# Optimization experiments

Hardware: AMD Instinct MI355X
Metric: run time of the kernel (lower is better)

The kernel has to match this reference:

```python
import jax, jax.numpy as jnp
import numpy as np

B, L, D, H = 4, 256, 512, 8
R = 64            # number of relative-position buckets
DK = D // H       # per-head dim


def setup_inputs() -> dict:
    key = jax.random.key(0)
    ks = jax.random.split(key, 16)
    s = 0.05
    inp = {
        "query": jax.random.normal(ks[0], (B, L, D), jnp.float32),
        "key": jax.random.normal(ks[1], (B, L, D), jnp.float32),
        "value": jax.random.normal(ks[2], (B, L, D), jnp.float32),
        "mask": jax.random.randint(ks[3], (B, L), 0, 2).astype(bool),
        "rel_pos": jax.random.randint(ks[4], (B, L, L), 0, R).astype(jnp.int32),
        "rel_q": jax.random.normal(ks[5], (H, R, DK), jnp.float32) * s,
        "rel_k": jax.random.normal(ks[6], (H, R, DK), jnp.float32) * s,
        "rel_v": jax.random.normal(ks[7], (B, L, L, D), jnp.float32) * s,
        "Wq": jax.random.normal(ks[8], (D, D), jnp.float32) * s,
        "bq": jnp.zeros((D,), jnp.float32),
        "Wk": jax.random.normal(ks[9], (D, D), jnp.float32) * s,
        "bk": jnp.zeros((D,), jnp.float32),
        "Wv": jax.random.normal(ks[10], (D, D), jnp.float32) * s,
        "bv": jnp.zeros((D,), jnp.float32),
        "Wo": jax.random.normal(ks[11], (D, D), jnp.float32) * s,
        "bo": jnp.zeros((D,), jnp.float32),
    }
    return inp


def _heads(x, W, b):
    # nn.Linear: x @ W^T + b, then split heads -> [B, H, L, DK]
    y = x @ W.T + b
    return y.reshape(x.shape[0], x.shape[1], H, DK).transpose(0, 2, 1, 3)


def reference(query, key, value, mask, rel_pos, rel_q, rel_k, rel_v,
              Wq, bq, Wk, bk, Wv, bv, Wo, bo):
    q = _heads(query, Wq, bq)   # [B,H,L,DK]
    k = _heads(key, Wk, bk)
    v = _heads(value, Wv, bv)

    rp = jnp.broadcast_to(rel_pos[:, None], (B, H, L, L))  # int index [B,H,L,L]

    scores = jnp.einsum('bhld,bhmd->bhlm', q, k)

    # content-to-position: gather over relative buckets
    c2p = jnp.einsum('bhld,hrd->bhlr', q, rel_k)            # [B,H,L,R]
    scores = scores + jnp.take_along_axis(c2p, rp, axis=-1)

    # position-to-content: gather with transposed index, then transpose back
    p2c = jnp.einsum('bhld,hrd->bhlr', k, rel_q)            # [B,H,L,R]
    p2c = jnp.take_along_axis(p2c, jnp.swapaxes(rp, -1, -2), axis=-1)
    scores = scores + jnp.swapaxes(p2c, -1, -2)

    scale_factor = 3.0  # 1 + c2p + p2c
    scores = scores / (scale_factor * np.sqrt(DK).astype(np.float32))
    scores = jnp.where(mask[:, None, None, :], jnp.float32(-1e9), scores)

    p = jax.nn.softmax(scores, axis=-1)  # dropout is identity in eval

    ctx = jnp.einsum('bhlm,bhmd->bhld', p, v)
    # rel_v contribution: rel_v -> [B,L,L,H,DK], contract over m (keys)
    rv = rel_v.reshape(B, L, L, H, DK)
    ctx = ctx + jnp.einsum('bhlm,blmhd->bhld', p, rv)

    out = ctx.transpose(0, 2, 1, 3).reshape(B, L, D)
    return out @ Wo.T + bo
```

## Files before the change

### kernel.cpp

```cpp
#include <hip/hip_runtime.h>
#include <hip/hip_bf16.h>
#include <math.h>

#define NB 4
#define NL 256
#define ND 512
#define NH 8
#define NR 64
#define NDK 64

typedef float f32x4 __attribute__((ext_vector_type(4)));
typedef short s16x8 __attribute__((ext_vector_type(8)));
typedef unsigned short u16;
typedef u16 u16x4 __attribute__((ext_vector_type(4)));

static __device__ __forceinline__ u16 f2bf(float f) {
    __hip_bfloat16 h = __float2bfloat16(f);
    return __builtin_bit_cast(unsigned short, h);
}

__global__ __launch_bounds__(256)
void convert_bf16_kernel(const float* __restrict__ q, const float* __restrict__ k,
                         const float* __restrict__ v, const float* __restrict__ wq,
                         const float* __restrict__ wk, const float* __restrict__ wv,
                         const float* __restrict__ wo,
                         u16* __restrict__ oq, u16* __restrict__ ok, u16* __restrict__ ov,
                         u16* __restrict__ owq, u16* __restrict__ owk,
                         u16* __restrict__ owv, u16* __restrict__ owo)
{
    const int job = blockIdx.y;
    const float* src; u16* dst; int n;
    switch (job) {
        case 0: src = q;  dst = oq;  n = 524288; break;
        case 1: src = k;  dst = ok;  n = 524288; break;
        case 2: src = v;  dst = ov;  n = 524288; break;
        case 3: src = wq; dst = owq; n = 262144; break;
        case 4: src = wk; dst = owk; n = 262144; break;
        case 5: src = wv; dst = owv; n = 262144; break;
        default: src = wo; dst = owo; n = 262144; break;
    }
    int idx = (blockIdx.x * 256 + threadIdx.x) * 4;
    if (idx >= n) return;
    f32x4 x = *(const f32x4*)&src[idx];
    u16x4 o;
    o.x = f2bf(x.x); o.y = f2bf(x.y); o.z = f2bf(x.z); o.w = f2bf(x.w);
    *(u16x4*)&dst[idx] = o;
}

__global__ __launch_bounds__(256)
void wprep_kernel(const float* __restrict__ Wq, const float* __restrict__ bq,
                  const float* __restrict__ Wk, const float* __restrict__ bk,
                  const float* __restrict__ RelK, const float* __restrict__ RelQ,
                  u16* __restrict__ W3, float* __restrict__ b3,
                  u16* __restrict__ W2, float* __restrict__ b2)
{
    const int z = blockIdx.y;
    const int t = threadIdx.x;

    if (z == 2) {
        if (blockIdx.x >= 2) return;
        const float* rel  = blockIdx.x ? RelQ : RelK;
        const float* bias = blockIdx.x ? bk : bq;
        float* out        = blockIdx.x ? b2 : b3;
        for (int hr = t; hr < 512; hr += 256) {
            int h = hr >> 6, r = hr & 63;
            float s = 0.f;
            #pragma unroll 8
            for (int d = 0; d < 64; ++d)
                s += rel[((size_t)h * NR + r) * NDK + d] * bias[h * 64 + d];
            out[hr] = s;
        }
        return;
    }

    const float* rel = z ? RelQ : RelK;
    const float* W   = z ? Wk : Wq;
    u16* Wout        = z ? W2 : W3;

    const int h  = blockIdx.x >> 3;
    const int e0 = (blockIdx.x & 7) * 64;

    __shared__ float At[64][68];
    __shared__ float Bs[64][68];

    const int ty = t >> 4, tx = t & 15;

    #pragma unroll
    for (int pass = 0; pass < 4; ++pass) {
        {
            int lr = t >> 2, lk = (t & 3) << 2;
            f32x4 a = *(const f32x4*)&rel[((size_t)h * NR + lr) * NDK + pass * 16 + lk];
            At[pass*16 + lk + 0][lr] = a.x; At[pass*16 + lk + 1][lr] = a.y;
            At[pass*16 + lk + 2][lr] = a.z; At[pass*16 + lk + 3][lr] = a.w;
        }
        {
            int dr = t >> 4, ec = (t & 15) << 2;
            *(f32x4*)&Bs[pass*16 + dr][ec] =
                *(const f32x4*)&W[(size_t)(h*64 + pass*16 + dr) * ND + e0 + ec];
        }
    }
    __syncthreads();

    float acc[4][4] = {{0.f,0.f,0.f,0.f},{0.f,0.f,0.f,0.f},
                       {0.f,0.f,0.f,0.f},{0.f,0.f,0.f,0.f}};
    #pragma unroll 16
    for (int kk = 0; kk < 64; ++kk) {
        f32x4 a4 = *(const f32x4*)&At[kk][ty*4];
        f32x4 b4 = *(const f32x4*)&Bs[kk][tx*4];
        #pragma unroll
        for (int i = 0; i < 4; ++i) {
            acc[i][0] += a4[i]*b4.x; acc[i][1] += a4[i]*b4.y;
            acc[i][2] += a4[i]*b4.z; acc[i][3] += a4[i]*b4.w;
        }
    }

    #pragma unroll
    for (int i = 0; i < 4; ++i) {
        u16x4 o;
        o.x = f2bf(acc[i][0]); o.y = f2bf(acc[i][1]);
        o.z = f2bf(acc[i][2]); o.w = f2bf(acc[i][3]);
        *(u16x4*)&Wout[(size_t)(h*64 + ty*4 + i) * ND + e0 + tx*4] = o;
    }
}

__global__ __launch_bounds__(256)
void gemm5_mfma_kernel(const u16* __restrict__ xq, const u16* __restrict__ xk,
                       const u16* __restrict__ xv,
                       const u16* __restrict__ wq, const u16* __restrict__ wk,
                       const u16* __restrict__ wv, const u16* __restrict__ w3,
                       const u16* __restrict__ w2,
                       const float* __restrict__ bq, const float* __restrict__ bk,
                       const float* __restrict__ bv, const float* __restrict__ b3,
                       const float* __restrict__ b2,
                       u16* __restrict__ qbf, u16* __restrict__ kbf,
                       float* __restrict__ v_ws, float* __restrict__ c2p,
                       float* __restrict__ p2c)
{
    const int z = blockIdx.z;
    const u16* __restrict__ X = (z==0 || z==3) ? xq : ((z==1 || z==4) ? xk : xv);
    const u16* __restrict__ W = (z==0)?wq:(z==1)?wk:(z==2)?wv:(z==3)?w3:w2;
    const float* __restrict__ bias = (z==0)?bq:(z==1)?bk:(z==2)?bv:(z==3)?b3:b2;

    const int t    = threadIdx.x;
    const int wv_  = t >> 6;
    const int lane = t & 63;
    const int lr   = lane & 15;
    const int kg   = lane >> 4;

    const int m0 = blockIdx.x * 64 + wv_ * 16;
    const int h  = blockIdx.y;
    const int n0 = h * 64;

    const u16* Ap = X + (size_t)(m0 + lr) * ND + kg * 8;
    const u16* Bp = W + (size_t)(n0 + lr) * ND + kg * 8;

    f32x4 acc[4] = {{0,0,0,0},{0,0,0,0},{0,0,0,0},{0,0,0,0}};

    for (int kt = 0; kt < 16; ++kt) {
        s16x8 a = *(const s16x8*)(Ap + kt * 32);
        #pragma unroll
        for (int nt = 0; nt < 4; ++nt) {
            s16x8 b = *(const s16x8*)(Bp + (size_t)nt * 16 * ND + kt * 32);
            acc[nt] = __builtin_amdgcn_mfma_f32_16x16x32_bf16(a, b, acc[nt], 0, 0, 0);
        }
    }

    #pragma unroll
    for (int nt = 0; nt < 4; ++nt) {
        const int col = n0 + nt * 16 + lr;
        const float bb = bias[col];
        #pragma unroll
        for (int r = 0; r < 4; ++r) {
            int row = m0 + kg * 4 + r;
            int bI  = row >> 8;
            int lI  = row & 255;
            size_t oidx = (((size_t)(bI * NH + h)) * NL + lI) * 64 + nt * 16 + lr;
            float val = acc[nt][r] + bb;
            if      (z == 0) qbf[oidx]  = f2bf(val);
            else if (z == 1) kbf[oidx]  = f2bf(val);
            else if (z == 2) v_ws[oidx] = val;
            else if (z == 3) c2p[oidx]  = val;
            else             p2c[oidx]  = val;
        }
    }
}

__global__ __launch_bounds__(512, 4)
void attn_ctx_kernel(const u16* __restrict__ qbf, const u16* __restrict__ kbf,
                     const float* __restrict__ Vws,
                     const float* __restrict__ C2P, const float* __restrict__ P2C,
                     const int* __restrict__ RelPos, const void* __restrict__ MaskP,
                     const float* __restrict__ RV, u16* __restrict__ CTXB)
{
    const int bh = blockIdx.y;
    const int b  = bh >> 3;
    const int h  = bh & 7;
    const int l0 = blockIdx.x * 16;
    const int t  = threadIdx.x;

    __shared__ float sc[16][257];
    __shared__ float cs[16][64];
    __shared__ float ps[32][68];
    __shared__ f32x4 redv[256];

    const unsigned char* mu = (const unsigned char*)MaskP;
    int loc1 = 0, loc23 = 0;
    if (t < 250) {
        loc1  = mu[t*4 + 1];
        loc23 = mu[t*4 + 2] | mu[t*4 + 3];
    }
    int any1  = __syncthreads_or(loc1);
    int any23 = __syncthreads_or(loc23);
    const int mlayout = any1 ? 0 : (any23 ? 1 : 2);

    if (t < 256)
        *(f32x4*)&cs[t >> 4][(t & 15) * 4] =
            *(const f32x4*)&C2P[(((size_t)bh * NL) + l0 + (t >> 4)) * NR + (t & 15) * 4];

    {
        const int wv_  = t >> 6;
        const int lane = t & 63;
        const int lr   = lane & 15;
        const int kg   = lane >> 4;
        const u16* Ap = qbf + ((size_t)bh * NL + l0 + lr) * 64 + kg * 8;
        s16x8 a0 = *(const s16x8*)Ap;
        s16x8 a1 = *(const s16x8*)(Ap + 32);
        #pragma unroll
        for (int c = 0; c < 2; ++c) {
            int m0 = wv_ * 32 + c * 16;
            const u16* Bp = kbf + ((size_t)bh * NL + m0 + lr) * 64 + kg * 8;
            s16x8 b0 = *(const s16x8*)Bp;
            s16x8 b1 = *(const s16x8*)(Bp + 32);
            f32x4 acc = {0.f, 0.f, 0.f, 0.f};
            acc = __builtin_amdgcn_mfma_f32_16x16x32_bf16(a0, b0, acc, 0, 0, 0);
            acc = __builtin_amdgcn_mfma_f32_16x16x32_bf16(a1, b1, acc, 0, 0, 0);
            #pragma unroll
            for (int r = 0; r < 4; ++r)
                sc[kg * 4 + r][m0 + lr] = acc[r];
        }
    }
    __syncthreads();

    const int i  = t >> 5;
    const int jj = t & 31;
    for (int mt = 0; mt < 8; ++mt) {
        *(f32x4*)&ps[t >> 4][(t & 15) * 4] =
            *(const f32x4*)&P2C[(((size_t)bh * NL) + mt * 32 + (t >> 4)) * NR + (t & 15) * 4];
        __syncthreads();

        const int m = mt * 32 + jj;
        int r = RelPos[((size_t)b * NL + l0 + i) * NL + m];
        float s = sc[i][m] + cs[i][r] + ps[jj][r];
        s *= (1.0f / 24.0f);

        float mval;
        if (mlayout == 0)      mval = (float)mu[b * NL + m];
        else if (mlayout == 1) mval = ((const float*)MaskP)[b * NL + m];
        else                   mval = (float)((const int*)MaskP)[b * NL + m];
        if (mval != 0.0f) s = -1e9f;

        __syncthreads();
        sc[i][m] = s;
        __syncthreads();
    }

    {
        float mx = -INFINITY;
        #pragma unroll
        for (int s32 = 0; s32 < 8; ++s32) mx = fmaxf(mx, sc[i][jj + 32*s32]);
        #pragma unroll
        for (int off = 16; off >= 1; off >>= 1) mx = fmaxf(mx, __shfl_xor(mx, off, 32));

        float sum = 0.f;
        float ev[8];
        #pragma unroll
        for (int s32 = 0; s32 < 8; ++s32) {
            ev[s32] = __expf(sc[i][jj + 32*s32] - mx);
            sum += ev[s32];
        }
        #pragma unroll
        for (int off = 16; off >= 1; off >>= 1) sum += __shfl_xor(sum, off, 32);
        float inv = 1.0f / sum;
        #pragma unroll
        for (int s32 = 0; s32 < 8; ++s32) sc[i][jj + 32*s32] = ev[s32] * inv;
    }
    __syncthreads();

    {
        const int half = t >> 8;
        const int di   = (t >> 4) & 15;
        const int d4   = t & 15;

        const float* rvp = RV + (((size_t)(b * NL + l0 + di)) * NL) * ND + h * 64 + d4 * 4;
        const float* vvp = Vws + ((size_t)(b * NH + h) * NL) * 64 + d4 * 4;

        f32x4 acc = {0.f, 0.f, 0.f, 0.f};
        #pragma unroll 4
        for (int m = half; m < NL; m += 2) {
            float w  = sc[di][m];
            f32x4 rv = __builtin_nontemporal_load((const f32x4*)(rvp + (size_t)m * ND));
            f32x4 vv = *(const f32x4*)(vvp + (size_t)m * 64);
            acc += w * (rv + vv);
        }

        if (half) redv[t & 255] = acc;
        __syncthreads();
        if (!half) {
            acc += redv[t];
            u16x4 o;
            o.x = f2bf(acc.x); o.y = f2bf(acc.y); o.z = f2bf(acc.z); o.w = f2bf(acc.w);
            *(u16x4*)&CTXB[((size_t)(b * NL + l0 + di)) * ND + h * 64 + d4 * 4] = o;
        }
    }
}

__global__ __launch_bounds__(256)
void out_proj_mfma_kernel(const u16* __restrict__ A, const u16* __restrict__ W,
                          const float* __restrict__ bias, float* __restrict__ C)
{
    const int t    = threadIdx.x;
    const int wv_  = t >> 6;
    const int lane = t & 63;
    const int lr   = lane & 15;
    const int kg   = lane >> 4;

    const int m0 = blockIdx.x * 32 + (wv_ & 1) * 16;
    const int n0 = blockIdx.y * 64 + (wv_ >> 1) * 32;

    const u16* Ap = A + (size_t)(m0 + lr) * ND + kg * 8;
    const u16* Bp = W + (size_t)(n0 + lr) * ND + kg * 8;

    f32x4 acc[2] = {{0,0,0,0},{0,0,0,0}};

    for (int kt = 0; kt < 16; ++kt) {
        s16x8 a = *(const s16x8*)(Ap + kt * 32);
        #pragma unroll
        for (int nt = 0; nt < 2; ++nt) {
            s16x8 b = *(const s16x8*)(Bp + (size_t)nt * 16 * ND + kt * 32);
            acc[nt] = __builtin_amdgcn_mfma_f32_16x16x32_bf16(a, b, acc[nt], 0, 0, 0);
        }
    }

    #pragma unroll
    for (int nt = 0; nt < 2; ++nt) {
        const int col = n0 + nt * 16 + lr;
        const float bb = bias[col];
        #pragma unroll
        for (int r = 0; r < 4; ++r) {
            int row = m0 + kg * 4 + r;
            C[(size_t)row * ND + col] = acc[nt][r] + bb;
        }
    }
}

extern "C" void kernel_launch(void* const* d_in, const int* in_sizes, int n_in,
                              void* d_out, int out_size, void* d_ws, size_t ws_size,
                              hipStream_t stream)
{
    const float* query   = (const float*)d_in[0];
    const float* key     = (const float*)d_in[1];
    const float* value   = (const float*)d_in[2];
    const void*  mask    = d_in[3];
    const int*   rel_pos = (const int*)d_in[4];
    const float* rel_q   = (const float*)d_in[5];
    const float* rel_k   = (const float*)d_in[6];
    const float* rel_v   = (const float*)d_in[7];
    const float* Wq = (const float*)d_in[8];
    const float* bq = (const float*)d_in[9];
    const float* Wk = (const float*)d_in[10];
    const float* bk = (const float*)d_in[11];
    const float* Wv = (const float*)d_in[12];
    const float* bv = (const float*)d_in[13];
    const float* Wo = (const float*)d_in[14];
    const float* bo = (const float*)d_in[15];

    float* wsf  = (float*)d_ws;
    float* v_ws = wsf;
    float* c2p  = v_ws + 524288;
    float* p2c  = c2p + 524288;
    float* b3   = p2c + 524288;
    float* b2   = b3 + 512;
    u16* wsu  = (u16*)(b2 + 512);
    u16* xqb  = wsu;
    u16* xkb  = xqb + 524288;
    u16* xvb  = xkb + 524288;
    u16* wqb  = xvb + 524288;
    u16* wkb  = wqb + 262144;
    u16* wvb  = wkb + 262144;
    u16* wob  = wvb + 262144;
    u16* w3b  = wob + 262144;
    u16* w2b  = w3b + 262144;
    u16* qbf  = w2b + 262144;
    u16* kbf  = qbf + 524288;
    u16* ctxb = kbf + 524288;

    convert_bf16_kernel<<<dim3(512, 7), 256, 0, stream>>>(
        query, key, value, Wq, Wk, Wv, Wo, xqb, xkb, xvb, wqb, wkb, wvb, wob);

    wprep_kernel<<<dim3(64, 3), 256, 0, stream>>>(
        Wq, bq, Wk, bk, rel_k, rel_q, w3b, b3, w2b, b2);

    gemm5_mfma_kernel<<<dim3(16, 8, 5), 256, 0, stream>>>(
        xqb, xkb, xvb, wqb, wkb, wvb, w3b, w2b,
        bq, bk, bv, b3, b2, qbf, kbf, v_ws, c2p, p2c);

    attn_ctx_kernel<<<dim3(16, 32), 512, 0, stream>>>(
        qbf, kbf, v_ws, c2p, p2c, rel_pos, mask, rel_v, ctxb);

    out_proj_mfma_kernel<<<dim3(32, 8), 256, 0, stream>>>(ctxb, wob, bo, (float*)d_out);
}
```

Before: 169.2 us.

## Fuse heads per attention block so rel_v rows are read once contiguously

Result: slower. 238.7 us (+41.1%).

```diff
diff --git a/kernel.cpp b/kernel.cpp
--- a/kernel.cpp
+++ b/kernel.cpp
@@ -13,10 +13,19 @@
 typedef short s16x8 __attribute__((ext_vector_type(8)));
 typedef unsigned short u16;
 typedef u16 u16x4 __attribute__((ext_vector_type(4)));
+typedef unsigned int u32;
+typedef u32 u32x2 __attribute__((ext_vector_type(2)));
+typedef u32 u32x4 __attribute__((ext_vector_type(4)));
 
 static __device__ __forceinline__ u16 f2bf(float f) {
     __hip_bfloat16 h = __float2bfloat16(f);
     return __builtin_bit_cast(unsigned short, h);
+}
+static __device__ __forceinline__ float bflo(u32 u) {
+    return __builtin_bit_cast(float, u << 16);
+}
+static __device__ __forceinline__ float bfhi(u32 u) {
+    return __builtin_bit_cast(float, u & 0xffff0000u);
 }
 
 __global__ __launch_bounds__(256)
@@ -133,8 +142,8 @@
                        const float* __restrict__ bv, const float* __restrict__ b3,
                        const float* __restrict__ b2,
                        u16* __restrict__ qbf, u16* __restrict__ kbf,
-                       float* __restrict__ v_ws, float* __restrict__ c2p,
-                       float* __restrict__ p2c)
+                       u16* __restrict__ vbf, float* __restrict__ c2p,
+                       u16* __restrict__ p2ct)
 {
     const int z = blockIdx.z;
     const u16* __restrict__ X = (z==0 || z==3) ? xq : ((z==1 || z==4) ? xk : xv);
@@ -174,34 +183,40 @@
             int row = m0 + kg * 4 + r;
             int bI  = row >> 8;
             int lI  = row & 255;
-            size_t oidx = (((size_t)(bI * NH + h)) * NL + lI) * 64 + nt * 16 + lr;
             float val = acc[nt][r] + bb;
-            if      (z == 0) qbf[oidx]  = f2bf(val);
-            else if (z == 1) kbf[oidx]  = f2bf(val);
-            else if (z == 2) v_ws[oidx] = val;
-            else if (z == 3) c2p[oidx]  = val;
-            else             p2c[oidx]  = val;
+            if (z == 4) {
+                p2ct[(((size_t)(bI * NL + lI)) * 64 + nt * 16 + lr) * 8 + h] = f2bf(val);
+            } else {
+                size_t oidx = (((size_t)(bI * NH + h)) * NL + lI) * 64 + nt * 16 + lr;
+                if      (z == 0) qbf[oidx] = f2bf(val);
+                else if (z == 1) kbf[oidx] = f2bf(val);
+                else if (z == 2) vbf[oidx] = f2bf(val);
+                else             c2p[oidx] = val;
+            }
         }
     }
 }
 
 __global__ __launch_bounds__(512, 4)
-void attn_ctx_kernel(const u16* __restrict__ qbf, const u16* __restrict__ kbf,
-                     const float* __restrict__ Vws,
-                     const float* __restrict__ C2P, const float* __restrict__ P2C,
-                     const int* __restrict__ RelPos, const void* __restrict__ MaskP,
-                     const float* __restrict__ RV, u16* __restrict__ CTXB)
-{
-    const int bh = blockIdx.y;
-    const int b  = bh >> 3;
-    const int h  = bh & 7;
-    const int l0 = blockIdx.x * 16;
-    const int t  = threadIdx.x;
-
-    __shared__ float sc[16][257];
-    __shared__ float cs[16][64];
-    __shared__ float ps[32][68];
-    __shared__ f32x4 redv[256];
+void attn_fused_kernel(const u16* __restrict__ qbf, const u16* __restrict__ kbf,
+                       const u16* __restrict__ vbf,
+                       const float* __restrict__ C2P, const u16* __restrict__ p2ct,
+                       const int* __restrict__ RelPos, const void* __restrict__ MaskP,
+                       const float* __restrict__ RV, u16* __restrict__ CTXB)
+{
+    const int bid  = blockIdx.x;
+    const int xcd  = bid & 7;
+    const int slot = bid >> 3;
+    const int b    = xcd >> 1;
+    const int l0   = (xcd & 1) * 128 + slot * 2;
+    const int t    = threadIdx.x;
+
+    __shared__ float sc[2][8][256];
+    __shared__ float qs[2][8][64];
+    __shared__ float cs[2][8][64];
+    __shared__ int   rp_lds[2][256];
+    __shared__ float maskv[256];
+    __shared__ f32x4 redv[2][128];
 
     const unsigned char* mu = (const unsigned char*)MaskP;
     int loc1 = 0, loc23 = 0;
@@ -213,61 +228,87 @@
     int any23 = __syncthreads_or(loc23);
     const int mlayout = any1 ? 0 : (any23 ? 1 : 2);
 
-    if (t < 256)
-        *(f32x4*)&cs[t >> 4][(t & 15) * 4] =
-            *(const f32x4*)&C2P[(((size_t)bh * NL) + l0 + (t >> 4)) * NR + (t & 15) * 4];
+    if (t < 256) {
+        int l = t >> 7, h = (t >> 4) & 7, d4 = t & 15;
+        u32x2 qw = *(const u32x2*)&qbf[(((size_t)(b*NH + h)) * NL + l0 + l) * 64 + d4*4];
+        qs[l][h][d4*4+0] = bflo(qw.x); qs[l][h][d4*4+1] = bfhi(qw.x);
+        qs[l][h][d4*4+2] = bflo(qw.y); qs[l][h][d4*4+3] = bfhi(qw.y);
+        *(f32x4*)&cs[l][h][d4*4] =
+            *(const f32x4*)&C2P[(((size_t)(b*NH + h)) * NL + l0 + l) * 64 + d4*4];
+        float mval;
+        if (mlayout == 0)      mval = (float)mu[b * NL + t];
+        else if (mlayout == 1) mval = ((const float*)MaskP)[b * NL + t];
+        else                   mval = (float)((const int*)MaskP)[b * NL + t];
+        maskv[t] = mval;
+    } else {
+        int tt = t - 256;
+        if (tt < 128) {
+            int l = tt >> 6, m4 = tt & 63;
+            *(int4*)&rp_lds[l][m4*4] =
+                *(const int4*)&RelPos[((size_t)b * NL + l0 + l) * NL + m4*4];
+        }
+    }
+    __syncthreads();
 
     {
-        const int wv_  = t >> 6;
-        const int lane = t & 63;
-        const int lr   = lane & 15;
-        const int kg   = lane >> 4;
-        const u16* Ap = qbf + ((size_t)bh * NL + l0 + lr) * 64 + kg * 8;
-        s16x8 a0 = *(const s16x8*)Ap;
-        s16x8 a1 = *(const s16x8*)(Ap + 32);
-        #pragma unroll
-        for (int c = 0; c < 2; ++c) {
-            int m0 = wv_ * 32 + c * 16;
-            const u16* Bp = kbf + ((size_t)bh * NL + m0 + lr) * 64 + kg * 8;
-            s16x8 b0 = *(const s16x8*)Bp;
-            s16x8 b1 = *(const s16x8*)(Bp + 32);
-            f32x4 acc = {0.f, 0.f, 0.f, 0.f};
-            acc = __builtin_amdgcn_mfma_f32_16x16x32_bf16(a0, b0, acc, 0, 0, 0);
-            acc = __builtin_amdgcn_mfma_f32_16x16x32_bf16(a1, b1, acc, 0, 0, 0);
+        const int h  = t >> 6;
+        const int m0 = (t & 63) * 4;
+        float acc[2][4] = {{0.f,0.f,0.f,0.f},{0.f,0.f,0.f,0.f}};
+        const u16* kr = kbf + (((size_t)(b*NH + h)) * NL + m0) * 64;
+        for (int c = 0; c < 8; ++c) {
+            f32x4 q00 = *(const f32x4*)&qs[0][h][c*8];
+            f32x4 q01 = *(const f32x4*)&qs[0][h][c*8+4];
+            f32x4 q10 = *(const f32x4*)&qs[1][h][c*8];
+            f32x4 q11 = *(const f32x4*)&qs[1][h][c*8+4];
             #pragma unroll
-            for (int r = 0; r < 4; ++r)
-                sc[kg * 4 + r][m0 + lr] = acc[r];
-        }
+            for (int i = 0; i < 4; ++i) {
+                u32x4 kw = *(const u32x4*)(kr + (size_t)i * 64 + c * 8);
+                float f0 = bflo(kw.x), f1 = bfhi(kw.x);
+                float f2 = bflo(kw.y), f3 = bfhi(kw.y);
+                float f4 = bflo(kw.z), f5 = bfhi(kw.z);
+                float f6 = bflo(kw.w), f7 = bfhi(kw.w);
+                acc[0][i] += f0*q00.x + f1*q00.y + f2*q00.z + f3*q00.w
+                           + f4*q01.x + f5*q01.y + f6*q01.z + f7*q01.w;
+                acc[1][i] += f0*q10.x + f1*q10.y + f2*q10.z + f3*q10.w
+                           + f4*q11.x + f5*q11.y + f6*q11.z + f7*q11.w;
+            }
+        }
+        f32x4 w0; w0.x = acc[0][0]; w0.y = acc[0][1]; w0.z = acc[0][2]; w0.w = acc[0][3];
+        f32x4 w1; w1.x = acc[1][0]; w1.y = acc[1][1]; w1.z = acc[1][2]; w1.w = acc[1][3];
+        *(f32x4*)&sc[0][h][m0] = w0;
+        *(f32x4*)&sc[1][h][m0] = w1;
     }
     __syncthreads();
 
-    const int i  = t >> 5;
-    const int jj = t & 31;
-    for (int mt = 0; mt < 8; ++mt) {
-        *(f32x4*)&ps[t >> 4][(t & 15) * 4] =
-            *(const f32x4*)&P2C[(((size_t)bh * NL) + mt * 32 + (t >> 4)) * NR + (t & 15) * 4];
-        __syncthreads();
-
-        const int m = mt * 32 + jj;
-        int r = RelPos[((size_t)b * NL + l0 + i) * NL + m];
-        float s = sc[i][m] + cs[i][r] + ps[jj][r];
-        s *= (1.0f / 24.0f);
-
-        float mval;
-        if (mlayout == 0)      mval = (float)mu[b * NL + m];
-        else if (mlayout == 1) mval = ((const float*)MaskP)[b * NL + m];
-        else                   mval = (float)((const int*)MaskP)[b * NL + m];
-        if (mval != 0.0f) s = -1e9f;
-
-        __syncthreads();
-        sc[i][m] = s;
-        __syncthreads();
-    }
-
     {
+        const int m  = t & 255;
+        const int hs = (t >> 8) * 4;
+        const float msk = maskv[m];
+        #pragma unroll
+        for (int l = 0; l < 2; ++l) {
+            int r = rp_lds[l][m];
+            u32x2 pw = *(const u32x2*)&p2ct[(((size_t)(b * NL + m)) * 64 + r) * 8 + hs];
+            float pv[4] = {bflo(pw.x), bfhi(pw.x), bflo(pw.y), bfhi(pw.y)};
+            #pragma unroll
+            for (int j = 0; j < 4; ++j) {
+                int hh = hs + j;
+                float s = sc[l][hh][m] + cs[l][hh][r] + pv[j];
+                s *= (1.0f / 24.0f);
+                if (msk != 0.0f) s = -1e9f;
+                sc[l][hh][m] = s;
+            }
+        }
+    }
+    __syncthreads();
+
+    {
+        const int row = t >> 5;
+        const int l   = row >> 3;
+        const int h   = row & 7;
+        const int jj  = t & 31;
         float mx = -INFINITY;
         #pragma unroll
-        for (int s32 = 0; s32 < 8; ++s32) mx = fmaxf(mx, sc[i][jj + 32*s32]);
+        for (int s32 = 0; s32 < 8; ++s32) mx = fmaxf(mx, sc[l][h][jj + 32*s32]);
         #pragma unroll
         for (int off = 16; off >= 1; off >>= 1) mx = fmaxf(mx, __shfl_xor(mx, off, 32));
 
@@ -275,41 +316,45 @@
         float ev[8];
         #pragma unroll
         for (int s32 = 0; s32 < 8; ++s32) {
-            ev[s32] = __expf(sc[i][jj + 32*s32] - mx);
+            ev[s32] = __expf(sc[l][h][jj + 32*s32] - mx);
             sum += ev[s32];
         }
         #pragma unroll
         for (int off = 16; off >= 1; off >>= 1) sum += __shfl_xor(sum, off, 32);
         float inv = 1.0f / sum;
         #pragma unroll
-        for (int s32 = 0; s32 < 8; ++s32) sc[i][jj + 32*s32] = ev[s32] * inv;
+        for (int s32 = 0; s32 < 8; ++s32) sc[l][h][jj + 32*s32] = ev[s32] * inv;
     }
     __syncthreads();
 
     {
-        const int half = t >> 8;
-        const int di   = (t >> 4) & 15;
-        const int d4   = t & 15;
-
-        const float* rvp = RV + (((size_t)(b * NL + l0 + di)) * NL) * ND + h * 64 + d4 * 4;
-        const float* vvp = Vws + ((size_t)(b * NH + h) * NL) * 64 + d4 * 4;
+        const int lgrp = t >> 8;
+        const int half = (t >> 7) & 1;
+        const int d4   = t & 127;
+        const int hD   = d4 >> 4;
+        const int dk4  = d4 & 15;
+
+        const float* rvp = RV + ((size_t)(b * NL + l0 + lgrp) * NL) * ND + d4 * 4;
+        const u16*   vvp = vbf + ((size_t)(b * NH + hD) * NL) * 64 + dk4 * 4;
 
         f32x4 acc = {0.f, 0.f, 0.f, 0.f};
         #pragma unroll 4
         for (int m = half; m < NL; m += 2) {
-            float w  = sc[di][m];
+            float w = sc[lgrp][hD][m];
             f32x4 rv = __builtin_nontemporal_load((const f32x4*)(rvp + (size_t)m * ND));
-            f32x4 vv = *(const f32x4*)(vvp + (size_t)m * 64);
+            u32x2 vw = *(const u32x2*)(vvp + (size_t)m * 64);
+            f32x4 vv;
+            vv.x = bflo(vw.x); vv.y = bfhi(vw.x); vv.z = bflo(vw.y); vv.w = bfhi(vw.y);
             acc += w * (rv + vv);
         }
 
-        if (half) redv[t & 255] = acc;
+        if (half) redv[lgrp][d4] = acc;
         __syncthreads();
         if (!half) {
-            acc += redv[t];
+            acc += redv[lgrp][d4];
             u16x4 o;
             o.x = f2bf(acc.x); o.y = f2bf(acc.y); o.z = f2bf(acc.z); o.w = f2bf(acc.w);
-            *(u16x4*)&CTXB[((size_t)(b * NL + l0 + di)) * ND + h * 64 + d4 * 4] = o;
+            *(u16x4*)&CTXB[((size_t)(b * NL + l0 + lgrp)) * ND + d4 * 4] = o;
         }
     }
 }
@@ -375,10 +420,8 @@
     const float* bo = (const float*)d_in[15];
 
     float* wsf  = (float*)d_ws;
-    float* v_ws = wsf;
-    float* c2p  = v_ws + 524288;
-    float* p2c  = c2p + 524288;
-    float* b3   = p2c + 524288;
+    float* c2p  = wsf;
+    float* b3   = c2p + 524288;
     float* b2   = b3 + 512;
     u16* wsu  = (u16*)(b2 + 512);
     u16* xqb  = wsu;
@@ -392,7 +435,9 @@
     u16* w2b  = w3b + 262144;
     u16* qbf  = w2b + 262144;
     u16* kbf  = qbf + 524288;
-    u16* ctxb = kbf + 524288;
+    u16* vbf  = kbf + 524288;
+    u16* p2ct = vbf + 524288;
+    u16* ctxb = p2ct + 524288;
 
     convert_bf16_kernel<<<dim3(512, 7), 256, 0, stream>>>(
         query, key, value, Wq, Wk, Wv, Wo, xqb, xkb, xvb, wqb, wkb, wvb, wob);
@@ -402,10 +447,10 @@
 
     gemm5_mfma_kernel<<<dim3(16, 8, 5), 256, 0, stream>>>(
         xqb, xkb, xvb, wqb, wkb, wvb, w3b, w2b,
-        bq, bk, bv, b3, b2, qbf, kbf, v_ws, c2p, p2c);
-
-    attn_ctx_kernel<<<dim3(16, 32), 512, 0, stream>>>(
-        qbf, kbf, v_ws, c2p, p2c, rel_pos, mask, rel_v, ctxb);
+        bq, bk, bv, b3, b2, qbf, kbf, vbf, c2p, p2ct);
+
+    attn_fused_kernel<<<dim3(512), 512, 0, stream>>>(
+        qbf, kbf, vbf, c2p, p2ct, rel_pos, mask, rel_v, ctxb);
 
     out_proj_mfma_kernel<<<dim3(32, 8), 256, 0, stream>>>(ctxb, wob, bo, (float*)d_out);
 }
```

## Fuse bf16 conversion into GEMMs and compute c2p/p2c inside attention kernel

Applied to the files above, without the earlier changes.

New measurement: 185.3 us. +9.5%, slower.

```diff
diff --git a/kernel.cpp b/kernel.cpp
--- a/kernel.cpp
+++ b/kernel.cpp
@@ -13,133 +13,40 @@
 typedef short s16x8 __attribute__((ext_vector_type(8)));
 typedef unsigned short u16;
 typedef u16 u16x4 __attribute__((ext_vector_type(4)));
+typedef u16 u16x8 __attribute__((ext_vector_type(8)));
+typedef unsigned int u32;
 
 static __device__ __forceinline__ u16 f2bf(float f) {
     __hip_bfloat16 h = __float2bfloat16(f);
     return __builtin_bit_cast(unsigned short, h);
 }
+static __device__ __forceinline__ float bf2f(u16 u) {
+    return __builtin_bit_cast(float, (u32)u << 16);
+}
+static __device__ __forceinline__ s16x8 loadcvt8(const float* __restrict__ p) {
+    f32x4 lo = *(const f32x4*)p;
+    f32x4 hi = *(const f32x4*)(p + 4);
+    s16x8 r;
+    r[0] = (short)f2bf(lo.x); r[1] = (short)f2bf(lo.y);
+    r[2] = (short)f2bf(lo.z); r[3] = (short)f2bf(lo.w);
+    r[4] = (short)f2bf(hi.x); r[5] = (short)f2bf(hi.y);
+    r[6] = (short)f2bf(hi.z); r[7] = (short)f2bf(hi.w);
+    return r;
+}
 
 __global__ __launch_bounds__(256)
-void convert_bf16_kernel(const float* __restrict__ q, const float* __restrict__ k,
-                         const float* __restrict__ v, const float* __restrict__ wq,
-                         const float* __restrict__ wk, const float* __restrict__ wv,
-                         const float* __restrict__ wo,
-                         u16* __restrict__ oq, u16* __restrict__ ok, u16* __restrict__ ov,
-                         u16* __restrict__ owq, u16* __restrict__ owk,
-                         u16* __restrict__ owv, u16* __restrict__ owo)
-{
-    const int job = blockIdx.y;
-    const float* src; u16* dst; int n;
-    switch (job) {
-        case 0: src = q;  dst = oq;  n = 524288; break;
-        case 1: src = k;  dst = ok;  n = 524288; break;
-        case 2: src = v;  dst = ov;  n = 524288; break;
-        case 3: src = wq; dst = owq; n = 262144; break;
-        case 4: src = wk; dst = owk; n = 262144; break;
-        case 5: src = wv; dst = owv; n = 262144; break;
-        default: src = wo; dst = owo; n = 262144; break;
-    }
-    int idx = (blockIdx.x * 256 + threadIdx.x) * 4;
-    if (idx >= n) return;
-    f32x4 x = *(const f32x4*)&src[idx];
-    u16x4 o;
-    o.x = f2bf(x.x); o.y = f2bf(x.y); o.z = f2bf(x.z); o.w = f2bf(x.w);
-    *(u16x4*)&dst[idx] = o;
-}
-
-__global__ __launch_bounds__(256)
-void wprep_kernel(const float* __restrict__ Wq, const float* __restrict__ bq,
-                  const float* __restrict__ Wk, const float* __restrict__ bk,
-                  const float* __restrict__ RelK, const float* __restrict__ RelQ,
-                  u16* __restrict__ W3, float* __restrict__ b3,
-                  u16* __restrict__ W2, float* __restrict__ b2)
-{
-    const int z = blockIdx.y;
-    const int t = threadIdx.x;
-
-    if (z == 2) {
-        if (blockIdx.x >= 2) return;
-        const float* rel  = blockIdx.x ? RelQ : RelK;
-        const float* bias = blockIdx.x ? bk : bq;
-        float* out        = blockIdx.x ? b2 : b3;
-        for (int hr = t; hr < 512; hr += 256) {
-            int h = hr >> 6, r = hr & 63;
-            float s = 0.f;
-            #pragma unroll 8
-            for (int d = 0; d < 64; ++d)
-                s += rel[((size_t)h * NR + r) * NDK + d] * bias[h * 64 + d];
-            out[hr] = s;
-        }
-        return;
-    }
-
-    const float* rel = z ? RelQ : RelK;
-    const float* W   = z ? Wk : Wq;
-    u16* Wout        = z ? W2 : W3;
-
-    const int h  = blockIdx.x >> 3;
-    const int e0 = (blockIdx.x & 7) * 64;
-
-    __shared__ float At[64][68];
-    __shared__ float Bs[64][68];
-
-    const int ty = t >> 4, tx = t & 15;
-
-    #pragma unroll
-    for (int pass = 0; pass < 4; ++pass) {
-        {
-            int lr = t >> 2, lk = (t & 3) << 2;
-            f32x4 a = *(const f32x4*)&rel[((size_t)h * NR + lr) * NDK + pass * 16 + lk];
-            At[pass*16 + lk + 0][lr] = a.x; At[pass*16 + lk + 1][lr] = a.y;
-            At[pass*16 + lk + 2][lr] = a.z; At[pass*16 + lk + 3][lr] = a.w;
-        }
-        {
-            int dr = t >> 4, ec = (t & 15) << 2;
-            *(f32x4*)&Bs[pass*16 + dr][ec] =
-                *(const f32x4*)&W[(size_t)(h*64 + pass*16 + dr) * ND + e0 + ec];
-        }
-    }
-    __syncthreads();
-
-    float acc[4][4] = {{0.f,0.f,0.f,0.f},{0.f,0.f,0.f,0.f},
-                       {0.f,0.f,0.f,0.f},{0.f,0.f,0.f,0.f}};
-    #pragma unroll 16
-    for (int kk = 0; kk < 64; ++kk) {
-        f32x4 a4 = *(const f32x4*)&At[kk][ty*4];
-        f32x4 b4 = *(const f32x4*)&Bs[kk][tx*4];
-        #pragma unroll
-        for (int i = 0; i < 4; ++i) {
-            acc[i][0] += a4[i]*b4.x; acc[i][1] += a4[i]*b4.y;
-            acc[i][2] += a4[i]*b4.z; acc[i][3] += a4[i]*b4.w;
-        }
-    }
-
-    #pragma unroll
-    for (int i = 0; i < 4; ++i) {
-        u16x4 o;
-        o.x = f2bf(acc[i][0]); o.y = f2bf(acc[i][1]);
-        o.z = f2bf(acc[i][2]); o.w = f2bf(acc[i][3]);
-        *(u16x4*)&Wout[(size_t)(h*64 + ty*4 + i) * ND + e0 + tx*4] = o;
-    }
-}
-
-__global__ __launch_bounds__(256)
-void gemm5_mfma_kernel(const u16* __restrict__ xq, const u16* __restrict__ xk,
-                       const u16* __restrict__ xv,
-                       const u16* __restrict__ wq, const u16* __restrict__ wk,
-                       const u16* __restrict__ wv, const u16* __restrict__ w3,
-                       const u16* __restrict__ w2,
-                       const float* __restrict__ bq, const float* __restrict__ bk,
-                       const float* __restrict__ bv, const float* __restrict__ b3,
-                       const float* __restrict__ b2,
+void gemm3_mfma_kernel(const float* __restrict__ Xq, const float* __restrict__ Xk,
+                       const float* __restrict__ Xv,
+                       const float* __restrict__ Wq, const float* __restrict__ bq,
+                       const float* __restrict__ Wk, const float* __restrict__ bk,
+                       const float* __restrict__ Wv, const float* __restrict__ bv,
                        u16* __restrict__ qbf, u16* __restrict__ kbf,
-                       float* __restrict__ v_ws, float* __restrict__ c2p,
-                       float* __restrict__ p2c)
+                       float* __restrict__ vws)
 {
     const int z = blockIdx.z;
-    const u16* __restrict__ X = (z==0 || z==3) ? xq : ((z==1 || z==4) ? xk : xv);
-    const u16* __restrict__ W = (z==0)?wq:(z==1)?wk:(z==2)?wv:(z==3)?w3:w2;
-    const float* __restrict__ bias = (z==0)?bq:(z==1)?bk:(z==2)?bv:(z==3)?b3:b2;
+    const float* __restrict__ X    = (z == 0) ? Xq : ((z == 1) ? Xk : Xv);
+    const float* __restrict__ W    = (z == 0) ? Wq : ((z == 1) ? Wk : Wv);
+    const float* __restrict__ bias = (z == 0) ? bq : ((z == 1) ? bk : bv);
 
     const int t    = threadIdx.x;
     const int wv_  = t >> 6;
@@ -147,60 +54,64 @@
     const int lr   = lane & 15;
     const int kg   = lane >> 4;
 
-    const int m0 = blockIdx.x * 64 + wv_ * 16;
     const int h  = blockIdx.y;
-    const int n0 = h * 64;
-
-    const u16* Ap = X + (size_t)(m0 + lr) * ND + kg * 8;
-    const u16* Bp = W + (size_t)(n0 + lr) * ND + kg * 8;
-
-    f32x4 acc[4] = {{0,0,0,0},{0,0,0,0},{0,0,0,0},{0,0,0,0}};
+    const int m0 = blockIdx.x * 32 + (wv_ & 1) * 16;
+    const int c0 = (wv_ >> 1) * 32;
+
+    const float* Ap = X + (size_t)(m0 + lr) * ND + kg * 8;
+    const float* Bp = W + (size_t)(h * 64 + c0 + lr) * ND + kg * 8;
+
+    f32x4 acc[2] = {{0,0,0,0},{0,0,0,0}};
 
     for (int kt = 0; kt < 16; ++kt) {
-        s16x8 a = *(const s16x8*)(Ap + kt * 32);
-        #pragma unroll
-        for (int nt = 0; nt < 4; ++nt) {
-            s16x8 b = *(const s16x8*)(Bp + (size_t)nt * 16 * ND + kt * 32);
+        s16x8 a = loadcvt8(Ap + kt * 32);
+        #pragma unroll
+        for (int nt = 0; nt < 2; ++nt) {
+            s16x8 b = loadcvt8(Bp + (size_t)nt * 16 * ND + kt * 32);
             acc[nt] = __builtin_amdgcn_mfma_f32_16x16x32_bf16(a, b, acc[nt], 0, 0, 0);
         }
     }
 
     #pragma unroll
-    for (int nt = 0; nt < 4; ++nt) {
-        const int col = n0 + nt * 16 + lr;
-        const float bb = bias[col];
+    for (int nt = 0; nt < 2; ++nt) {
+        const int off = c0 + nt * 16 + lr;
+        const float bb = bias[h * 64 + off];
         #pragma unroll
         for (int r = 0; r < 4; ++r) {
             int row = m0 + kg * 4 + r;
             int bI  = row >> 8;
             int lI  = row & 255;
-            size_t oidx = (((size_t)(bI * NH + h)) * NL + lI) * 64 + nt * 16 + lr;
+            size_t oidx = (((size_t)(bI * NH + h)) * NL + lI) * 64 + off;
             float val = acc[nt][r] + bb;
-            if      (z == 0) qbf[oidx]  = f2bf(val);
-            else if (z == 1) kbf[oidx]  = f2bf(val);
-            else if (z == 2) v_ws[oidx] = val;
-            else if (z == 3) c2p[oidx]  = val;
-            else             p2c[oidx]  = val;
+            if      (z == 0) qbf[oidx] = f2bf(val);
+            else if (z == 1) kbf[oidx] = f2bf(val);
+            else             vws[oidx] = val;
         }
     }
 }
 
 __global__ __launch_bounds__(512, 4)
-void attn_ctx_kernel(const u16* __restrict__ qbf, const u16* __restrict__ kbf,
-                     const float* __restrict__ Vws,
-                     const float* __restrict__ C2P, const float* __restrict__ P2C,
-                     const int* __restrict__ RelPos, const void* __restrict__ MaskP,
-                     const float* __restrict__ RV, u16* __restrict__ CTXB)
+void attn_fused_kernel(const u16* __restrict__ qbf, const u16* __restrict__ kbf,
+                       const float* __restrict__ vws,
+                       const float* __restrict__ RelK, const float* __restrict__ RelQ,
+                       const int* __restrict__ RelPos, const void* __restrict__ MaskP,
+                       const float* __restrict__ RV, u16* __restrict__ CTXB)
 {
-    const int bh = blockIdx.y;
-    const int b  = bh >> 3;
-    const int h  = bh & 7;
-    const int l0 = blockIdx.x * 16;
-    const int t  = threadIdx.x;
+    const int bid  = blockIdx.x;
+    const int xcd  = bid & 7;
+    const int idx  = bid >> 3;
+    const int b    = xcd >> 1;
+    const int lhalf= xcd & 1;
+    const int h    = idx & 7;
+    const int lt   = idx >> 3;
+    const int l0   = lhalf * 128 + lt * 16;
+    const int bh   = b * NH + h;
+    const int t    = threadIdx.x;
 
     __shared__ float sc[16][257];
     __shared__ float cs[16][64];
-    __shared__ float ps[32][68];
+    __shared__ u16   psall[256][64];
+    __shared__ float maskv[256];
     __shared__ f32x4 redv[256];
 
     const unsigned char* mu = (const unsigned char*)MaskP;
@@ -213,18 +124,24 @@
     int any23 = __syncthreads_or(loc23);
     const int mlayout = any1 ? 0 : (any23 ? 1 : 2);
 
-    if (t < 256)
-        *(f32x4*)&cs[t >> 4][(t & 15) * 4] =
-            *(const f32x4*)&C2P[(((size_t)bh * NL) + l0 + (t >> 4)) * NR + (t & 15) * 4];
+    if (t < 256) {
+        float mval;
+        if (mlayout == 0)      mval = (float)mu[b * NL + t];
+        else if (mlayout == 1) mval = ((const float*)MaskP)[b * NL + t];
+        else                   mval = (float)((const int*)MaskP)[b * NL + t];
+        maskv[t] = mval;
+    }
 
     {
         const int wv_  = t >> 6;
         const int lane = t & 63;
         const int lr   = lane & 15;
         const int kg   = lane >> 4;
+
         const u16* Ap = qbf + ((size_t)bh * NL + l0 + lr) * 64 + kg * 8;
         s16x8 a0 = *(const s16x8*)Ap;
         s16x8 a1 = *(const s16x8*)(Ap + 32);
+
         #pragma unroll
         for (int c = 0; c < 2; ++c) {
             int m0 = wv_ * 32 + c * 16;
@@ -238,51 +155,80 @@
             for (int r = 0; r < 4; ++r)
                 sc[kg * 4 + r][m0 + lr] = acc[r];
         }
+
+        if (wv_ < 4) {
+            const int rt = wv_;
+            const float* Rp = RelK + ((size_t)h * NR + rt * 16 + lr) * NDK + kg * 8;
+            s16x8 rb0 = loadcvt8(Rp);
+            s16x8 rb1 = loadcvt8(Rp + 32);
+            f32x4 acc = {0.f, 0.f, 0.f, 0.f};
+            acc = __builtin_amdgcn_mfma_f32_16x16x32_bf16(a0, rb0, acc, 0, 0, 0);
+            acc = __builtin_amdgcn_mfma_f32_16x16x32_bf16(a1, rb1, acc, 0, 0, 0);
+            #pragma unroll
+            for (int r = 0; r < 4; ++r)
+                cs[kg * 4 + r][rt * 16 + lr] = acc[r];
+        }
+
+        s16x8 qb0[4], qb1[4];
+        #pragma unroll
+        for (int rt = 0; rt < 4; ++rt) {
+            const float* Rp = RelQ + ((size_t)h * NR + rt * 16 + lr) * NDK + kg * 8;
+            qb0[rt] = loadcvt8(Rp);
+            qb1[rt] = loadcvt8(Rp + 32);
+        }
+        #pragma unroll
+        for (int mi = 0; mi < 2; ++mi) {
+            const int mt = wv_ * 2 + mi;
+            const u16* Kp = kbf + ((size_t)bh * NL + mt * 16 + lr) * 64 + kg * 8;
+            s16x8 ka0 = *(const s16x8*)Kp;
+            s16x8 ka1 = *(const s16x8*)(Kp + 32);
+            #pragma unroll
+            for (int rt = 0; rt < 4; ++rt) {
+                f32x4 acc = {0.f, 0.f, 0.f, 0.f};
+                acc = __builtin_amdgcn_mfma_f32_16x16x32_bf16(ka0, qb0[rt], acc, 0, 0, 0);
+                acc = __builtin_amdgcn_mfma_f32_16x16x32_bf16(ka1, qb1[rt], acc, 0, 0, 0);
+                #pragma unroll
+                for (int r = 0; r < 4; ++r)
+                    psall[mt * 16 + kg * 4 + r][rt * 16 + lr] = f2bf(acc[r]);
+            }
+        }
     }
     __syncthreads();
 
     const int i  = t >> 5;
     const int jj = t & 31;
-    for (int mt = 0; mt < 8; ++mt) {
-        *(f32x4*)&ps[t >> 4][(t & 15) * 4] =
-            *(const f32x4*)&P2C[(((size_t)bh * NL) + mt * 32 + (t >> 4)) * NR + (t & 15) * 4];
-        __syncthreads();
-
-        const int m = mt * 32 + jj;
-        int r = RelPos[((size_t)b * NL + l0 + i) * NL + m];
-        float s = sc[i][m] + cs[i][r] + ps[jj][r];
-        s *= (1.0f / 24.0f);
-
-        float mval;
-        if (mlayout == 0)      mval = (float)mu[b * NL + m];
-        else if (mlayout == 1) mval = ((const float*)MaskP)[b * NL + m];
-        else                   mval = (float)((const int*)MaskP)[b * NL + m];
-        if (mval != 0.0f) s = -1e9f;
-
-        __syncthreads();
-        sc[i][m] = s;
-        __syncthreads();
+    {
+        const size_t rowbase = ((size_t)b * NL + l0 + i) * NL;
+        #pragma unroll
+        for (int s = 0; s < 8; ++s) {
+            const int m = s * 32 + jj;
+            int r = RelPos[rowbase + m];
+            float val = sc[i][m] + cs[i][r] + bf2f(psall[m][r]);
+            val *= (1.0f / 24.0f);
+            if (maskv[m] != 0.0f) val = -1e9f;
+            sc[i][m] = val;
+        }
     }
 
     {
         float mx = -INFINITY;
         #pragma unroll
-        for (int s32 = 0; s32 < 8; ++s32) mx = fmaxf(mx, sc[i][jj + 32*s32]);
+        for (int s = 0; s < 8; ++s) mx = fmaxf(mx, sc[i][jj + 32*s]);
         #pragma unroll
         for (int off = 16; off >= 1; off >>= 1) mx = fmaxf(mx, __shfl_xor(mx, off, 32));
 
         float sum = 0.f;
         float ev[8];
         #pragma unroll
-        for (int s32 = 0; s32 < 8; ++s32) {
-            ev[s32] = __expf(sc[i][jj + 32*s32] - mx);
-            sum += ev[s32];
+        for (int s = 0; s < 8; ++s) {
+            ev[s] = __expf(sc[i][jj + 32*s] - mx);
+            sum += ev[s];
         }
         #pragma unroll
         for (int off = 16; off >= 1; off >>= 1) sum += __shfl_xor(sum, off, 32);
         float inv = 1.0f / sum;
         #pragma unroll
-        for (int s32 = 0; s32 < 8; ++s32) sc[i][jj + 32*s32] = ev[s32] * inv;
+        for (int s = 0; s < 8; ++s) sc[i][jj + 32*s] = ev[s] * inv;
     }
     __syncthreads();
 
@@ -292,7 +238,7 @@
         const int d4   = t & 15;
 
         const float* rvp = RV + (((size_t)(b * NL + l0 + di)) * NL) * ND + h * 64 + d4 * 4;
-        const float* vvp = Vws + ((size_t)(b * NH + h) * NL) * 64 + d4 * 4;
+        const float* vvp = vws + ((size_t)bh * NL) * 64 + d4 * 4;
 
         f32x4 acc = {0.f, 0.f, 0.f, 0.f};
         #pragma unroll 4
@@ -315,7 +261,7 @@
 }
 
 __global__ __launch_bounds__(256)
-void out_proj_mfma_kernel(const u16* __restrict__ A, const u16* __restrict__ W,
+void out_proj_mfma_kernel(const u16* __restrict__ A, const float* __restrict__ Wo,
                           const float* __restrict__ bias, float* __restrict__ C)
 {
     const int t    = threadIdx.x;
@@ -324,32 +270,26 @@
     const int lr   = lane & 15;
     const int kg   = lane >> 4;
 
-    const int m0 = blockIdx.x * 32 + (wv_ & 1) * 16;
-    const int n0 = blockIdx.y * 64 + (wv_ >> 1) * 32;
-
-    const u16* Ap = A + (size_t)(m0 + lr) * ND + kg * 8;
-    const u16* Bp = W + (size_t)(n0 + lr) * ND + kg * 8;
-
-    f32x4 acc[2] = {{0,0,0,0},{0,0,0,0}};
+    const int m0 = blockIdx.x * 16;
+    const int n0 = blockIdx.y * 64 + wv_ * 16;
+
+    const u16*   Ap = A  + (size_t)(m0 + lr) * ND + kg * 8;
+    const float* Bp = Wo + (size_t)(n0 + lr) * ND + kg * 8;
+
+    f32x4 acc = {0.f, 0.f, 0.f, 0.f};
 
     for (int kt = 0; kt < 16; ++kt) {
         s16x8 a = *(const s16x8*)(Ap + kt * 32);
-        #pragma unroll
-        for (int nt = 0; nt < 2; ++nt) {
-            s16x8 b = *(const s16x8*)(Bp + (size_t)nt * 16 * ND + kt * 32);
-            acc[nt] = __builtin_amdgcn_mfma_f32_16x16x32_bf16(a, b, acc[nt], 0, 0, 0);
-        }
-    }
-
+        s16x8 b = loadcvt8(Bp + kt * 32);
+        acc = __builtin_amdgcn_mfma_f32_16x16x32_bf16(a, b, acc, 0, 0, 0);
+    }
+
+    const int col = n0 + lr;
+    const float bb = bias[col];
     #pragma unroll
-    for (int nt = 0; nt < 2; ++nt) {
-        const int col = n0 + nt * 16 + lr;
-        const float bb = bias[col];
-        #pragma unroll
-        for (int r = 0; r < 4; ++r) {
-            int row = m0 + kg * 4 + r;
-            C[(size_t)row * ND + col] = acc[nt][r] + bb;
-        }
+    for (int r = 0; r < 4; ++r) {
+        int row = m0 + kg * 4 + r;
+        C[(size_t)row * ND + col] = acc[r] + bb;
     }
 }
 
@@ -374,38 +314,17 @@
     const float* Wo = (const float*)d_in[14];
     const float* bo = (const float*)d_in[15];
 
-    float* wsf  = (float*)d_ws;
-    float* v_ws = wsf;
-    float* c2p  = v_ws + 524288;
-    float* p2c  = c2p + 524288;
-    float* b3   = p2c + 524288;
-    float* b2   = b3 + 512;
-    u16* wsu  = (u16*)(b2 + 512);
-    u16* xqb  = wsu;
-    u16* xkb  = xqb + 524288;
-    u16* xvb  = xkb + 524288;
-    u16* wqb  = xvb + 524288;
-    u16* wkb  = wqb + 262144;
-    u16* wvb  = wkb + 262144;
-    u16* wob  = wvb + 262144;
-    u16* w3b  = wob + 262144;
-    u16* w2b  = w3b + 262144;
-    u16* qbf  = w2b + 262144;
+    float* vws  = (float*)d_ws;
+    u16* qbf  = (u16*)(vws + 524288);
     u16* kbf  = qbf + 524288;
     u16* ctxb = kbf + 524288;
 
-    convert_bf16_kernel<<<dim3(512, 7), 256, 0, stream>>>(
-        query, key, value, Wq, Wk, Wv, Wo, xqb, xkb, xvb, wqb, wkb, wvb, wob);
-
-    wprep_kernel<<<dim3(64, 3), 256, 0, stream>>>(
-        Wq, bq, Wk, bk, rel_k, rel_q, w3b, b3, w2b, b2);
-
-    gemm5_mfma_kernel<<<dim3(16, 8, 5), 256, 0, stream>>>(
-        xqb, xkb, xvb, wqb, wkb, wvb, w3b, w2b,
-        bq, bk, bv, b3, b2, qbf, kbf, v_ws, c2p, p2c);
-
-    attn_ctx_kernel<<<dim3(16, 32), 512, 0, stream>>>(
-        qbf, kbf, v_ws, c2p, p2c, rel_pos, mask, rel_v, ctxb);
-
-    out_proj_mfma_kernel<<<dim3(32, 8), 256, 0, stream>>>(ctxb, wob, bo, (float*)d_out);
-}
+    gemm3_mfma_kernel<<<dim3(32, 8, 3), 256, 0, stream>>>(
+        query, key, value, Wq, bq, Wk, bk, Wv, bv, qbf, kbf, vws);
+
+    attn_fused_kernel<<<dim3(512), 512, 0, stream>>>(
+        qbf, kbf, vws, rel_k, rel_q, rel_pos, mask, rel_v, ctxb);
+
+    out_proj_mfma_kernel<<<dim3(64, 8), 256, 0, stream>>>(
+        ctxb, Wo, bo, (float*)d_out);
+}
```
